# Kernel optimization log

Measured on AMD Instinct MI355X. Metric: run time of the kernel, lower is better.

Reference implementation:

```python
import jax, jax.numpy as jnp
import numpy as np

N_NODES = 100000
N_EDGES = 800000
IN_FEATS = 64
HIDDEN = 128
OUT_FEATS = 64
BN_EPS = 1e-5


def setup_inputs() -> dict:
    key = jax.random.key(0)
    ks = jax.random.split(key, 10)
    x = jax.random.normal(ks[0], (N_NODES, IN_FEATS), dtype=jnp.float32)
    edge_src = jax.random.randint(ks[1], (N_EDGES,), 0, N_NODES, dtype=jnp.int64)
    edge_dst = jax.random.randint(ks[2], (N_EDGES,), 0, N_NODES, dtype=jnp.int64)
    def lin(k, fan_in, fan_out):
        return jax.random.normal(k, (fan_in, fan_out), dtype=jnp.float32) / np.sqrt(fan_in)
    return {
        "x": x,
        "edge_src": edge_src,
        "edge_dst": edge_dst,
        "W_self1": lin(ks[3], IN_FEATS, HIDDEN),
        "W_neigh1": lin(ks[4], IN_FEATS, HIDDEN),
        "b1": jnp.zeros((HIDDEN,), jnp.float32),
        "bn_gamma": jnp.ones((HIDDEN,), jnp.float32),
        "bn_beta": jnp.zeros((HIDDEN,), jnp.float32),
        "W_self2": lin(ks[5], HIDDEN, OUT_FEATS),
        "W_neigh2": lin(ks[6], HIDDEN, OUT_FEATS),
        "b2": jnp.zeros((OUT_FEATS,), jnp.float32),
    }


def _sage_mean(h, edge_src, edge_dst, W_self, W_neigh, b, n_nodes):
    # mean aggregation over in-edges (SpMM): gather src feats, segment-sum by dst
    msg = h[edge_src]                                              # [E, F]
    summed = jax.ops.segment_sum(msg, edge_dst, num_segments=n_nodes)
    deg = jax.ops.segment_sum(jnp.ones(edge_dst.shape, h.dtype), edge_dst,
                              num_segments=n_nodes)
    agg = summed / jnp.maximum(deg, 1.0)[:, None]                  # zero-degree -> 0
    return h @ W_self + agg @ W_neigh + b


def reference(x, edge_src, edge_dst, W_self1, W_neigh1, b1, bn_gamma, bn_beta,
              W_self2, W_neigh2, b2):
    n = x.shape[0]
    h = _sage_mean(x, edge_src, edge_dst, W_self1, W_neigh1, b1, n)   # [N, hidden]
    # BatchNorm1d over the node dimension (training-mode batch stats)
    mu = jnp.mean(h, axis=0)
    var = jnp.var(h, axis=0)
    h = bn_gamma * (h - mu) * jax.lax.rsqrt(var + BN_EPS) + bn_beta
    h = jax.nn.relu(h)                                                # dropout = identity (eval)
    return _sage_mean(h, edge_src, edge_dst, W_self2, W_neigh2, b2, n)
```

## Files before the change

kernel.cpp:

```cpp
#include <hip/hip_runtime.h>

#define N_NODES 100000
#define N_EDGES 800000
#define IN_F 64
#define HID 128
#define OUT_F 64
#define BN_EPS 1e-5f
#define SCAN_NBLK ((N_NODES + 255) / 256)

typedef __attribute__((ext_vector_type(8))) short short8v;
typedef __attribute__((ext_vector_type(4))) float f32x4;

static __device__ __forceinline__ unsigned short f2bf(float f) {
  unsigned u = __float_as_uint(f);
  return (unsigned short)((u + 0x7FFFu + ((u >> 16) & 1u)) >> 16);
}
static __device__ __forceinline__ float bflo(unsigned u) {
  return __uint_as_float(u << 16);
}
static __device__ __forceinline__ float bfhi(unsigned u) {
  return __uint_as_float(u & 0xFFFF0000u);
}

__global__ __launch_bounds__(256) void cvtzero_kernel(
    const float* __restrict__ x, unsigned short* __restrict__ xb,
    int* __restrict__ cursor) {
  int t = blockIdx.x * 256 + threadIdx.x;
  if (t < N_NODES / 4) {
    int4 z = {0, 0, 0, 0};
    reinterpret_cast<int4*>(cursor)[t] = z;
  }
  if (t >= N_NODES * IN_F / 8) return;
  float4 a = reinterpret_cast<const float4*>(x)[t * 2];
  float4 b = reinterpret_cast<const float4*>(x)[t * 2 + 1];
  uint4 o;
  o.x = (unsigned)f2bf(a.x) | ((unsigned)f2bf(a.y) << 16);
  o.y = (unsigned)f2bf(a.z) | ((unsigned)f2bf(a.w) << 16);
  o.z = (unsigned)f2bf(b.x) | ((unsigned)f2bf(b.y) << 16);
  o.w = (unsigned)f2bf(b.z) | ((unsigned)f2bf(b.w) << 16);
  reinterpret_cast<uint4*>(xb)[t] = o;
}

__global__ __launch_bounds__(256) void pass1_kernel(
    const int* __restrict__ edst, int* __restrict__ cursor,
    unsigned short* __restrict__ pos16) {
  int t = blockIdx.x * 256 + threadIdx.x;
  if (t >= N_EDGES / 4) return;
  int4 d = reinterpret_cast<const int4*>(edst)[t];
  ushort4 p;
  p.x = (unsigned short)atomicAdd(cursor + d.x, 1);
  p.y = (unsigned short)atomicAdd(cursor + d.y, 1);
  p.z = (unsigned short)atomicAdd(cursor + d.z, 1);
  p.w = (unsigned short)atomicAdd(cursor + d.w, 1);
  reinterpret_cast<ushort4*>(pos16)[t] = p;
}

__global__ __launch_bounds__(256) void blocksum_kernel(
    const int* __restrict__ degi, int* __restrict__ bsum) {
  __shared__ int ls[256];
  int i = blockIdx.x * 256 + threadIdx.x;
  ls[threadIdx.x] = (i < N_NODES) ? degi[i] : 0;
  __syncthreads();
  for (int off = 128; off > 0; off >>= 1) {
    if (threadIdx.x < off) ls[threadIdx.x] += ls[threadIdx.x + off];
    __syncthreads();
  }
  if (threadIdx.x == 0) bsum[blockIdx.x] = ls[0];
}

__global__ __launch_bounds__(512) void scanb_kernel(
    const int* __restrict__ bsum, int* __restrict__ boff,
    int* __restrict__ rowstart, float* __restrict__ bnsum) {
  __shared__ int ls[512];
  int t = threadIdx.x;
  if (t < 256) bnsum[t] = 0.f;
  int v = (t < SCAN_NBLK) ? bsum[t] : 0;
  ls[t] = v;
  __syncthreads();
  for (int off = 1; off < 512; off <<= 1) {
    int u = (t >= off) ? ls[t - off] : 0;
    __syncthreads();
    ls[t] += u;
    __syncthreads();
  }
  if (t < SCAN_NBLK) boff[t] = ls[t] - v;
  if (t == 511) rowstart[N_NODES] = ls[511];
}

__global__ __launch_bounds__(256) void writerow_kernel(
    const int* __restrict__ degi, const int* __restrict__ boff,
    int* __restrict__ rowstart) {
  __shared__ int ls[256];
  int i = blockIdx.x * 256 + threadIdx.x;
  int t = threadIdx.x;
  int v = (i < N_NODES) ? degi[i] : 0;
  ls[t] = v;
  __syncthreads();
  for (int off = 1; off < 256; off <<= 1) {
    int u = (t >= off) ? ls[t - off] : 0;
    __syncthreads();
    ls[t] += u;
    __syncthreads();
  }
  if (i < N_NODES) rowstart[i] = boff[blockIdx.x] + ls[t] - v;
}

__global__ __launch_bounds__(256) void scatter_kernel(
    const int* __restrict__ esrc, const int* __restrict__ edst,
    const unsigned short* __restrict__ pos16,
    const int* __restrict__ rowstart, int* __restrict__ csr) {
  int t = blockIdx.x * 256 + threadIdx.x;
  if (t >= N_EDGES / 4) return;
  int4 s = reinterpret_cast<const int4*>(esrc)[t];
  int4 d = reinterpret_cast<const int4*>(edst)[t];
  ushort4 p = reinterpret_cast<const ushort4*>(pos16)[t];
  csr[rowstart[d.x] + p.x] = s.x;
  csr[rowstart[d.y] + p.y] = s.y;
  csr[rowstart[d.z] + p.z] = s.z;
  csr[rowstart[d.w] + p.w] = s.w;
}

__global__ __launch_bounds__(512) void gemm1_fused(
    const unsigned short* __restrict__ xb, const int* __restrict__ rowstart,
    const int* __restrict__ csr, const float* __restrict__ Ws,
    const float* __restrict__ Wn, const float* __restrict__ b,
    unsigned short* __restrict__ hb) {
  __shared__ __align__(16) unsigned short wt[128 * 128];
  __shared__ __align__(16) unsigned short aggl[128][72];
  __shared__ float bs[HID];
  int tid = threadIdx.x;
  for (int i = tid; i < 128 * 128; i += 512) {
    int k = i >> 7, j = i & 127;
    float v = (k < 64) ? Ws[k * HID + j] : Wn[(k - 64) * HID + j];
    int idx = (j << 7) | k;
    wt[idx ^ ((j & 15) << 3)] = f2bf(v);
  }
  if (tid < HID) bs[tid] = b[tid];
  __syncthreads();

  {
    int r_local = tid >> 2;
    int jj = tid & 3;
    int row = blockIdx.x * 128 + r_local;
    float acc[16];
#pragma unroll
    for (int e = 0; e < 16; ++e) acc[e] = 0.f;
    if (row < N_NODES) {
      int r0 = rowstart[row];
      int r1 = rowstart[row + 1];
      int i = r0;
      for (; i + 3 < r1; i += 4) {
        int s0 = csr[i], s1 = csr[i + 1], s2 = csr[i + 2], s3 = csr[i + 3];
        const uint4* p0 =
            reinterpret_cast<const uint4*>(xb + (size_t)s0 * 64 + jj * 16);
        const uint4* p1 =
            reinterpret_cast<const uint4*>(xb + (size_t)s1 * 64 + jj * 16);
        const uint4* p2 =
            reinterpret_cast<const uint4*>(xb + (size_t)s2 * 64 + jj * 16);
        const uint4* p3 =
            reinterpret_cast<const uint4*>(xb + (size_t)s3 * 64 + jj * 16);
        uint4 a0 = p0[0], b0 = p0[1];
        uint4 a1 = p1[0], b1 = p1[1];
        uint4 a2 = p2[0], b2 = p2[1];
        uint4 a3 = p3[0], b3 = p3[1];
        acc[0] += (bflo(a0.x) + bflo(a1.x)) + (bflo(a2.x) + bflo(a3.x));
        acc[1] += (bfhi(a0.x) + bfhi(a1.x)) + (bfhi(a2.x) + bfhi(a3.x));
        acc[2] += (bflo(a0.y) + bflo(a1.y)) + (bflo(a2.y) + bflo(a3.y));
        acc[3] += (bfhi(a0.y) + bfhi(a1.y)) + (bfhi(a2.y) + bfhi(a3.y));
        acc[4] += (bflo(a0.z) + bflo(a1.z)) + (bflo(a2.z) + bflo(a3.z));
        acc[5] += (bfhi(a0.z) + bfhi(a1.z)) + (bfhi(a2.z) + bfhi(a3.z));
        acc[6] += (bflo(a0.w) + bflo(a1.w)) + (bflo(a2.w) + bflo(a3.w));
        acc[7] += (bfhi(a0.w) + bfhi(a1.w)) + (bfhi(a2.w) + bfhi(a3.w));
        acc[8] += (bflo(b0.x) + bflo(b1.x)) + (bflo(b2.x) + bflo(b3.x));
        acc[9] += (bfhi(b0.x) + bfhi(b1.x)) + (bfhi(b2.x) + bfhi(b3.x));
        acc[10] += (bflo(b0.y) + bflo(b1.y)) + (bflo(b2.y) + bflo(b3.y));
        acc[11] += (bfhi(b0.y) + bfhi(b1.y)) + (bfhi(b2.y) + bfhi(b3.y));
        acc[12] += (bflo(b0.z) + bflo(b1.z)) + (bflo(b2.z) + bflo(b3.z));
        acc[13] += (bfhi(b0.z) + bfhi(b1.z)) + (bfhi(b2.z) + bfhi(b3.z));
        acc[14] += (bflo(b0.w) + bflo(b1.w)) + (bflo(b2.w) + bflo(b3.w));
        acc[15] += (bfhi(b0.w) + bfhi(b1.w)) + (bfhi(b2.w) + bfhi(b3.w));
      }
      for (; i < r1; ++i) {
        int s0 = csr[i];
        const uint4* p0 =
            reinterpret_cast<const uint4*>(xb + (size_t)s0 * 64 + jj * 16);
        uint4 a0 = p0[0], b0 = p0[1];
        acc[0] += bflo(a0.x);
        acc[1] += bfhi(a0.x);
        acc[2] += bflo(a0.y);
        acc[3] += bfhi(a0.y);
        acc[4] += bflo(a0.z);
        acc[5] += bfhi(a0.z);
        acc[6] += bflo(a0.w);
        acc[7] += bfhi(a0.w);
        acc[8] += bflo(b0.x);
        acc[9] += bfhi(b0.x);
        acc[10] += bflo(b0.y);
        acc[11] += bfhi(b0.y);
        acc[12] += bflo(b0.z);
        acc[13] += bfhi(b0.z);
        acc[14] += bflo(b0.w);
        acc[15] += bfhi(b0.w);
      }
      int deg = r1 - r0;
      float rd = 1.0f / (float)(deg > 0 ? deg : 1);
#pragma unroll
      for (int e = 0; e < 16; ++e) acc[e] *= rd;
    }
    uint4 o0, o1;
    o0.x = (unsigned)f2bf(acc[0]) | ((unsigned)f2bf(acc[1]) << 16);
    o0.y = (unsigned)f2bf(acc[2]) | ((unsigned)f2bf(acc[3]) << 16);
    o0.z = (unsigned)f2bf(acc[4]) | ((unsigned)f2bf(acc[5]) << 16);
    o0.w = (unsigned)f2bf(acc[6]) | ((unsigned)f2bf(acc[7]) << 16);
    o1.x = (unsigned)f2bf(acc[8]) | ((unsigned)f2bf(acc[9]) << 16);
    o1.y = (unsigned)f2bf(acc[10]) | ((unsigned)f2bf(acc[11]) << 16);
    o1.z = (unsigned)f2bf(acc[12]) | ((unsigned)f2bf(acc[13]) << 16);
    o1.w = (unsigned)f2bf(acc[14]) | ((unsigned)f2bf(acc[15]) << 16);
    uint4* dst = reinterpret_cast<uint4*>(&aggl[r_local][jj * 16]);
    dst[0] = o0;
    dst[1] = o1;
  }
  asm volatile("s_waitcnt lgkmcnt(0)" ::: "memory");

  int wave = tid >> 6, lane = tid & 63;
  int m = lane & 15, kg = lane >> 4;
  int rbase = blockIdx.x * 128 + wave * 16;
  int rowa = rbase + m;
  if (rowa >= N_NODES) rowa = N_NODES - 1;
  int lr = wave * 16 + m;

  short8v a[4];
#pragma unroll
  for (int kt = 0; kt < 4; ++kt) {
    int c0 = kt * 32 + kg * 8;
    if (c0 < 64) {
      a[kt] = *reinterpret_cast<const short8v*>(xb + (size_t)rowa * 64 + c0);
    } else {
      a[kt] = *reinterpret_cast<const short8v*>(&aggl[lr][c0 - 64]);
    }
  }

  f32x4 acc[8];
#pragma unroll
  for (int nt = 0; nt < 8; ++nt) acc[nt] = (f32x4){0.f, 0.f, 0.f, 0.f};

#pragma unroll
  for (int nt = 0; nt < 8; ++nt) {
    int col = nt * 16 + m;
    int base = col << 7;
    int sw = (col & 15) << 3;
#pragma unroll
    for (int kt = 0; kt < 4; ++kt) {
      int idx = (base | (kt * 32 + kg * 8)) ^ sw;
      short8v bf = *reinterpret_cast<const short8v*>(&wt[idx]);
      acc[nt] = __builtin_amdgcn_mfma_f32_16x16x32_bf16(a[kt], bf, acc[nt], 0, 0, 0);
    }
  }

#pragma unroll
  for (int nt = 0; nt < 8; ++nt) {
    int col = nt * 16 + m;
    float bias = bs[col];
#pragma unroll
    for (int r = 0; r < 4; ++r) {
      int rr = rbase + kg * 4 + r;
      if (rr < N_NODES) hb[(size_t)rr * HID + col] = f2bf(acc[nt][r] + bias);
    }
  }
}

__global__ __launch_bounds__(256) void aggb2_kernel(
    const unsigned short* __restrict__ zb, const unsigned short* __restrict__ sb,
    const int* __restrict__ rowstart, const int* __restrict__ csr,
    float* __restrict__ out) {
  int n = blockIdx.x * 32 + (threadIdx.x >> 3);
  int j = threadIdx.x & 7;
  if (n >= N_NODES) return;
  int r0 = rowstart[n];
  int r1 = rowstart[n + 1];
  float acc[8] = {0.f, 0.f, 0.f, 0.f, 0.f, 0.f, 0.f, 0.f};
  int i = r0;
  for (; i + 3 < r1; i += 4) {
    int s0 = csr[i], s1 = csr[i + 1], s2 = csr[i + 2], s3 = csr[i + 3];
    uint4 v0 = *reinterpret_cast<const uint4*>(zb + (size_t)s0 * 64 + j * 8);
    uint4 v1 = *reinterpret_cast<const uint4*>(zb + (size_t)s1 * 64 + j * 8);
    uint4 v2 = *reinterpret_cast<const uint4*>(zb + (size_t)s2 * 64 + j * 8);
    uint4 v3 = *reinterpret_cast<const uint4*>(zb + (size_t)s3 * 64 + j * 8);
    acc[0] += (bflo(v0.x) + bflo(v1.x)) + (bflo(v2.x) + bflo(v3.x));
    acc[1] += (bfhi(v0.x) + bfhi(v1.x)) + (bfhi(v2.x) + bfhi(v3.x));
    acc[2] += (bflo(v0.y) + bflo(v1.y)) + (bflo(v2.y) + bflo(v3.y));
    acc[3] += (bfhi(v0.y) + bfhi(v1.y)) + (bfhi(v2.y) + bfhi(v3.y));
    acc[4] += (bflo(v0.z) + bflo(v1.z)) + (bflo(v2.z) + bflo(v3.z));
    acc[5] += (bfhi(v0.z) + bfhi(v1.z)) + (bfhi(v2.z) + bfhi(v3.z));
    acc[6] += (bflo(v0.w) + bflo(v1.w)) + (bflo(v2.w) + bflo(v3.w));
    acc[7] += (bfhi(v0.w) + bfhi(v1.w)) + (bfhi(v2.w) + bfhi(v3.w));
  }
  for (; i < r1; ++i) {
    int s0 = csr[i];
    uint4 v0 = *reinterpret_cast<const uint4*>(zb + (size_t)s0 * 64 + j * 8);
    acc[0] += bflo(v0.x);
    acc[1] += bfhi(v0.x);
    acc[2] += bflo(v0.y);
    acc[3] += bfhi(v0.y);
    acc[4] += bflo(v0.z);
    acc[5] += bfhi(v0.z);
    acc[6] += bflo(v0.w);
    acc[7] += bfhi(v0.w);
  }
  int deg = r1 - r0;
  float rd = 1.0f / (float)(deg > 0 ? deg : 1);
  uint4 sv = *reinterpret_cast<const uint4*>(sb + (size_t)n * 64 + j * 8);
  float* dp = out + (size_t)n * 64 + j * 8;
  __builtin_nontemporal_store(bflo(sv.x) + acc[0] * rd, dp + 0);
  __builtin_nontemporal_store(bfhi(sv.x) + acc[1] * rd, dp + 1);
  __builtin_nontemporal_store(bflo(sv.y) + acc[2] * rd, dp + 2);
  __builtin_nontemporal_store(bfhi(sv.y) + acc[3] * rd, dp + 3);
  __builtin_nontemporal_store(bflo(sv.z) + acc[4] * rd, dp + 4);
  __builtin_nontemporal_store(bfhi(sv.z) + acc[5] * rd, dp + 5);
  __builtin_nontemporal_store(bflo(sv.w) + acc[6] * rd, dp + 6);
  __builtin_nontemporal_store(bfhi(sv.w) + acc[7] * rd, dp + 7);
}

__global__ __launch_bounds__(256) void bnstats_kernel(
    const unsigned short* __restrict__ hb, float* __restrict__ bnsum) {
  int j = threadIdx.x & 15;
  int g = threadIdx.x >> 4;
  float s[8] = {0.f, 0.f, 0.f, 0.f, 0.f, 0.f, 0.f, 0.f};
  float q[8] = {0.f, 0.f, 0.f, 0.f, 0.f, 0.f, 0.f, 0.f};
  for (int r = blockIdx.x * 16 + g; r < N_NODES; r += gridDim.x * 16) {
    uint4 v = *reinterpret_cast<const uint4*>(hb + (size_t)r * HID + j * 8);
    float f0 = bflo(v.x), f1 = bfhi(v.x), f2 = bflo(v.y), f3 = bfhi(v.y);
    float f4 = bflo(v.z), f5 = bfhi(v.z), f6 = bflo(v.w), f7 = bfhi(v.w);
    s[0] += f0; q[0] += f0 * f0;
    s[1] += f1; q[1] += f1 * f1;
    s[2] += f2; q[2] += f2 * f2;
    s[3] += f3; q[3] += f3 * f3;
    s[4] += f4; q[4] += f4 * f4;
    s[5] += f5; q[5] += f5 * f5;
    s[6] += f6; q[6] += f6 * f6;
    s[7] += f7; q[7] += f7 * f7;
  }
  __shared__ float lss[256 * 8];
  __shared__ float lqq[256 * 8];
#pragma unroll
  for (int e = 0; e < 8; ++e) {
    lss[threadIdx.x * 8 + e] = s[e];
    lqq[threadIdx.x * 8 + e] = q[e];
  }
  __syncthreads();
  if (threadIdx.x < 128) {
    int f = threadIdx.x;
    int jj = f >> 3, e = f & 7;
    float S = 0.f, Q = 0.f;
#pragma unroll
    for (int gg = 0; gg < 16; ++gg) {
      S += lss[(gg * 16 + jj) * 8 + e];
      Q += lqq[(gg * 16 + jj) * 8 + e];
    }
    unsafeAtomicAdd(bnsum + f, S);
    unsafeAtomicAdd(bnsum + 128 + f, Q);
  }
}

__global__ __launch_bounds__(512) void gemm2_mfma(
    const unsigned short* __restrict__ hb, const float* __restrict__ bnsum,
    const float* __restrict__ gamma, const float* __restrict__ beta,
    const float* __restrict__ Wn, const float* __restrict__ Ws,
    const float* __restrict__ b, unsigned short* __restrict__ zb,
    unsigned short* __restrict__ sb) {
  __shared__ __align__(16) unsigned short wt[128 * 128];
  __shared__ float scs[HID];
  __shared__ float shs[HID];
  __shared__ float bz[OUT_F];
  int tid = threadIdx.x;
  for (int i = tid; i < 128 * 128; i += 512) {
    int k = i >> 7, j = i & 127;
    float v = (j < 64) ? Wn[k * OUT_F + j] : Ws[k * OUT_F + (j - 64)];
    int idx = (j << 7) | k;
    wt[idx ^ ((j & 15) << 3)] = f2bf(v);
  }
  if (tid < HID) {
    const float invn = 1.0f / (float)N_NODES;
    float mu = bnsum[tid] * invn;
    float var = bnsum[128 + tid] * invn - mu * mu;
    float sc = gamma[tid] * rsqrtf(var + BN_EPS);
    scs[tid] = sc;
    shs[tid] = beta[tid] - mu * sc;
  }
  if (tid < OUT_F) bz[tid] = b[tid];
  __syncthreads();

  int wave = tid >> 6, lane = tid & 63;
  int m = lane & 15, kg = lane >> 4;
  int rbase = blockIdx.x * 128 + wave * 16;
  int rowa = rbase + m;
  if (rowa >= N_NODES) rowa = N_NODES - 1;

  short8v a[4];
#pragma unroll
  for (int kt = 0; kt < 4; ++kt) {
    int c0 = kt * 32 + kg * 8;
    uint4 raw = *reinterpret_cast<const uint4*>(hb + (size_t)rowa * HID + c0);
    float4 sc0 = *reinterpret_cast<const float4*>(&scs[c0]);
    float4 sc1 = *reinterpret_cast<const float4*>(&scs[c0 + 4]);
    float4 sh0 = *reinterpret_cast<const float4*>(&shs[c0]);
    float4 sh1 = *reinterpret_cast<const float4*>(&shs[c0 + 4]);
    short8v av;
    av[0] = (short)f2bf(fmaxf(bflo(raw.x) * sc0.x + sh0.x, 0.f));
    av[1] = (short)f2bf(fmaxf(bfhi(raw.x) * sc0.y + sh0.y, 0.f));
    av[2] = (short)f2bf(fmaxf(bflo(raw.y) * sc0.z + sh0.z, 0.f));
    av[3] = (short)f2bf(fmaxf(bfhi(raw.y) * sc0.w + sh0.w, 0.f));
    av[4] = (short)f2bf(fmaxf(bflo(raw.z) * sc1.x + sh1.x, 0.f));
    av[5] = (short)f2bf(fmaxf(bfhi(raw.z) * sc1.y + sh1.y, 0.f));
    av[6] = (short)f2bf(fmaxf(bflo(raw.w) * sc1.z + sh1.z, 0.f));
    av[7] = (short)f2bf(fmaxf(bfhi(raw.w) * sc1.w + sh1.w, 0.f));
    a[kt] = av;
  }

  f32x4 acc[8];
#pragma unroll
  for (int nt = 0; nt < 8; ++nt) acc[nt] = (f32x4){0.f, 0.f, 0.f, 0.f};

#pragma unroll
  for (int nt = 0; nt < 8; ++nt) {
    int col = nt * 16 + m;
    int base = col << 7;
    int sw = (col & 15) << 3;
#pragma unroll
    for (int kt = 0; kt < 4; ++kt) {
      int idx = (base | (kt * 32 + kg * 8)) ^ sw;
      short8v bf = *reinterpret_cast<const short8v*>(&wt[idx]);
      acc[nt] = __builtin_amdgcn_mfma_f32_16x16x32_bf16(a[kt], bf, acc[nt], 0, 0, 0);
    }
  }

#pragma unroll
  for (int nt = 0; nt < 8; ++nt) {
    int col = nt * 16 + m;
#pragma unroll
    for (int r = 0; r < 4; ++r) {
      int rr = rbase + kg * 4 + r;
      if (rr < N_NODES) {
        float v = acc[nt][r];
        if (col < 64)
          zb[(size_t)rr * OUT_F + col] = f2bf(v);
        else
          sb[(size_t)rr * OUT_F + (col - 64)] = f2bf(v + bz[col - 64]);
      }
    }
  }
}

extern "C" void kernel_launch(void* const* d_in, const int* in_sizes, int n_in,
                              void* d_out, int out_size, void* d_ws,
                              size_t ws_size, hipStream_t stream) {
  const float* x = (const float*)d_in[0];
  const int* esrc = (const int*)d_in[1];
  const int* edst = (const int*)d_in[2];
  const float* Ws1 = (const float*)d_in[3];
  const float* Wn1 = (const float*)d_in[4];
  const float* b1 = (const float*)d_in[5];
  const float* gamma = (const float*)d_in[6];
  const float* beta = (const float*)d_in[7];
  const float* Ws2 = (const float*)d_in[8];
  const float* Wn2 = (const float*)d_in[9];
  const float* b2 = (const float*)d_in[10];
  float* out = (float*)d_out;

  float* ws = (float*)d_ws;
  float* bnsum = ws;
  int* cursor = (int*)(ws + 512);
  int* rowstart = cursor + N_NODES;
  int* bsum = rowstart + N_NODES + 1;
  int* boff = bsum + SCAN_NBLK;
  int* csr = boff + SCAN_NBLK;
  int pos16_off = ((512 + 2 * N_NODES + 1 + 2 * SCAN_NBLK + N_EDGES) + 3) & ~3;
  unsigned short* pos16 = (unsigned short*)(ws + pos16_off);
  unsigned short* xb = (unsigned short*)(ws + pos16_off + N_EDGES / 2);
  unsigned short* zbuf = xb + (size_t)N_NODES * 64;
  unsigned short* sb = zbuf + (size_t)N_NODES * 64;
  unsigned short* hb = sb + (size_t)N_NODES * 64;

  const int e4grid = (N_EDGES / 4 + 255) / 256;
  cvtzero_kernel<<<(N_NODES * IN_F / 8 + 255) / 256, 256, 0, stream>>>(x, xb,
                                                                       cursor);
  pass1_kernel<<<e4grid, 256, 0, stream>>>(edst, cursor, pos16);
  blocksum_kernel<<<SCAN_NBLK, 256, 0, stream>>>(cursor, bsum);
  scanb_kernel<<<1, 512, 0, stream>>>(bsum, boff, rowstart, bnsum);
  writerow_kernel<<<SCAN_NBLK, 256, 0, stream>>>(cursor, boff, rowstart);
  scatter_kernel<<<e4grid, 256, 0, stream>>>(esrc, edst, pos16, rowstart, csr);

  const int ggrid = (N_NODES + 127) / 128;
  const int agrid = (N_NODES + 31) / 32;
  gemm1_fused<<<ggrid, 512, 0, stream>>>(xb, rowstart, csr, Ws1, Wn1, b1, hb);

  bnstats_kernel<<<256, 256, 0, stream>>>(hb, bnsum);

  gemm2_mfma<<<ggrid, 512, 0, stream>>>(hb, bnsum, gamma, beta, Wn2, Ws2, b2,
                                        zbuf, sb);
  aggb2_kernel<<<agrid, 256, 0, stream>>>(zbuf, sb, rowstart, csr, out);
}
```

Measured before the change: 175.8 us.

## Pre-convert weights to bf16 once and read B fragments from global

Weight transposition and bf16 conversion for both layers move into the prep kernel, which writes compact column-major bf16 weight tables to the workspace. The GEMM kernels no longer stage the 32KB weight tile into LDS per block; MFMA B operands are loaded straight from global/L2. Blocks shrink to 256 threads and 64 rows, which lowers LDS use and may raise occupancy. The cost is repeated global loads of weights per block, relying on cache hits, and twice as many blocks.

```diff
diff --git a/kernel.cpp b/kernel.cpp
--- a/kernel.cpp
+++ b/kernel.cpp
@@ -22,23 +22,48 @@
   return __uint_as_float(u & 0xFFFF0000u);
 }
 
-__global__ __launch_bounds__(256) void cvtzero_kernel(
-    const float* __restrict__ x, unsigned short* __restrict__ xb,
+__global__ __launch_bounds__(256) void prep_kernel(
+    const float* __restrict__ x, const float* __restrict__ Ws1,
+    const float* __restrict__ Wn1, const float* __restrict__ Wn2,
+    const float* __restrict__ Ws2, unsigned short* __restrict__ xb,
+    unsigned short* __restrict__ wb1, unsigned short* __restrict__ wb2,
     int* __restrict__ cursor) {
   int t = blockIdx.x * 256 + threadIdx.x;
   if (t < N_NODES / 4) {
     int4 z = {0, 0, 0, 0};
     reinterpret_cast<int4*>(cursor)[t] = z;
   }
-  if (t >= N_NODES * IN_F / 8) return;
-  float4 a = reinterpret_cast<const float4*>(x)[t * 2];
-  float4 b = reinterpret_cast<const float4*>(x)[t * 2 + 1];
-  uint4 o;
-  o.x = (unsigned)f2bf(a.x) | ((unsigned)f2bf(a.y) << 16);
-  o.y = (unsigned)f2bf(a.z) | ((unsigned)f2bf(a.w) << 16);
-  o.z = (unsigned)f2bf(b.x) | ((unsigned)f2bf(b.y) << 16);
-  o.w = (unsigned)f2bf(b.z) | ((unsigned)f2bf(b.w) << 16);
-  reinterpret_cast<uint4*>(xb)[t] = o;
+  if (t < N_NODES * IN_F / 8) {
+    float4 a = reinterpret_cast<const float4*>(x)[t * 2];
+    float4 b = reinterpret_cast<const float4*>(x)[t * 2 + 1];
+    uint4 o;
+    o.x = (unsigned)f2bf(a.x) | ((unsigned)f2bf(a.y) << 16);
+    o.y = (unsigned)f2bf(a.z) | ((unsigned)f2bf(a.w) << 16);
+    o.z = (unsigned)f2bf(b.x) | ((unsigned)f2bf(b.y) << 16);
+    o.w = (unsigned)f2bf(b.z) | ((unsigned)f2bf(b.w) << 16);
+    reinterpret_cast<uint4*>(xb)[t] = o;
+  } else {
+    int idx = t - N_NODES * IN_F / 8;
+    if (idx < 4096) {
+      int e0 = idx * 8;
+      int table = e0 >> 14;
+      int ee0 = e0 & 16383;
+      int col = ee0 >> 7, k0 = ee0 & 127;
+      unsigned short tmp[8];
+#pragma unroll
+      for (int q = 0; q < 8; ++q) {
+        int k = k0 + q;
+        float v;
+        if (table == 0)
+          v = (k < 64) ? Ws1[k * HID + col] : Wn1[(k - 64) * HID + col];
+        else
+          v = (col < 64) ? Wn2[k * OUT_F + col] : Ws2[k * OUT_F + (col - 64)];
+        tmp[q] = f2bf(v);
+      }
+      unsigned short* dst = (table == 0 ? wb1 : wb2) + ee0;
+      *reinterpret_cast<uint4*>(dst) = *reinterpret_cast<const uint4*>(tmp);
+    }
+  }
 }
 
 __global__ __launch_bounds__(256) void pass1_kernel(
@@ -120,28 +145,17 @@
   csr[rowstart[d.w] + p.w] = s.w;
 }
 
-__global__ __launch_bounds__(512) void gemm1_fused(
+__global__ __launch_bounds__(256) void gemm1_fused(
     const unsigned short* __restrict__ xb, const int* __restrict__ rowstart,
-    const int* __restrict__ csr, const float* __restrict__ Ws,
-    const float* __restrict__ Wn, const float* __restrict__ b,
-    unsigned short* __restrict__ hb) {
-  __shared__ __align__(16) unsigned short wt[128 * 128];
-  __shared__ __align__(16) unsigned short aggl[128][72];
-  __shared__ float bs[HID];
+    const int* __restrict__ csr, const unsigned short* __restrict__ wb,
+    const float* __restrict__ b, unsigned short* __restrict__ hb) {
+  __shared__ __align__(16) unsigned short aggl[64][72];
   int tid = threadIdx.x;
-  for (int i = tid; i < 128 * 128; i += 512) {
-    int k = i >> 7, j = i & 127;
-    float v = (k < 64) ? Ws[k * HID + j] : Wn[(k - 64) * HID + j];
-    int idx = (j << 7) | k;
-    wt[idx ^ ((j & 15) << 3)] = f2bf(v);
-  }
-  if (tid < HID) bs[tid] = b[tid];
-  __syncthreads();
 
   {
     int r_local = tid >> 2;
     int jj = tid & 3;
-    int row = blockIdx.x * 128 + r_local;
+    int row = blockIdx.x * 64 + r_local;
     float acc[16];
 #pragma unroll
     for (int e = 0; e < 16; ++e) acc[e] = 0.f;
@@ -224,7 +238,7 @@
 
   int wave = tid >> 6, lane = tid & 63;
   int m = lane & 15, kg = lane >> 4;
-  int rbase = blockIdx.x * 128 + wave * 16;
+  int rbase = blockIdx.x * 64 + wave * 16;
   int rowa = rbase + m;
   if (rowa >= N_NODES) rowa = N_NODES - 1;
   int lr = wave * 16 + m;
@@ -247,12 +261,11 @@
 #pragma unroll
   for (int nt = 0; nt < 8; ++nt) {
     int col = nt * 16 + m;
-    int base = col << 7;
-    int sw = (col & 15) << 3;
+    const unsigned short* wcol = wb + ((size_t)col << 7);
 #pragma unroll
     for (int kt = 0; kt < 4; ++kt) {
-      int idx = (base | (kt * 32 + kg * 8)) ^ sw;
-      short8v bf = *reinterpret_cast<const short8v*>(&wt[idx]);
+      short8v bf =
+          *reinterpret_cast<const short8v*>(wcol + kt * 32 + kg * 8);
       acc[nt] = __builtin_amdgcn_mfma_f32_16x16x32_bf16(a[kt], bf, acc[nt], 0, 0, 0);
     }
   }
@@ -260,7 +273,7 @@
 #pragma unroll
   for (int nt = 0; nt < 8; ++nt) {
     int col = nt * 16 + m;
-    float bias = bs[col];
+    float bias = b[col];
 #pragma unroll
     for (int r = 0; r < 4; ++r) {
       int rr = rbase + kg * 4 + r;
@@ -362,23 +375,14 @@
   }
 }
 
-__global__ __launch_bounds__(512) void gemm2_mfma(
+__global__ __launch_bounds__(256) void gemm2_mfma(
     const unsigned short* __restrict__ hb, const float* __restrict__ bnsum,
     const float* __restrict__ gamma, const float* __restrict__ beta,
-    const float* __restrict__ Wn, const float* __restrict__ Ws,
-    const float* __restrict__ b, unsigned short* __restrict__ zb,
-    unsigned short* __restrict__ sb) {
-  __shared__ __align__(16) unsigned short wt[128 * 128];
+    const unsigned short* __restrict__ wb, const float* __restrict__ b,
+    unsigned short* __restrict__ zb, unsigned short* __restrict__ sb) {
   __shared__ float scs[HID];
   __shared__ float shs[HID];
-  __shared__ float bz[OUT_F];
   int tid = threadIdx.x;
-  for (int i = tid; i < 128 * 128; i += 512) {
-    int k = i >> 7, j = i & 127;
-    float v = (j < 64) ? Wn[k * OUT_F + j] : Ws[k * OUT_F + (j - 64)];
-    int idx = (j << 7) | k;
-    wt[idx ^ ((j & 15) << 3)] = f2bf(v);
-  }
   if (tid < HID) {
     const float invn = 1.0f / (float)N_NODES;
     float mu = bnsum[tid] * invn;
@@ -387,12 +391,11 @@
     scs[tid] = sc;
     shs[tid] = beta[tid] - mu * sc;
   }
-  if (tid < OUT_F) bz[tid] = b[tid];
   __syncthreads();
 
   int wave = tid >> 6, lane = tid & 63;
   int m = lane & 15, kg = lane >> 4;
-  int rbase = blockIdx.x * 128 + wave * 16;
+  int rbase = blockIdx.x * 64 + wave * 16;
   int rowa = rbase + m;
   if (rowa >= N_NODES) rowa = N_NODES - 1;
 
@@ -424,12 +427,11 @@
 #pragma unroll
   for (int nt = 0; nt < 8; ++nt) {
     int col = nt * 16 + m;
-    int base = col << 7;
-    int sw = (col & 15) << 3;
+    const unsigned short* wcol = wb + ((size_t)col << 7);
 #pragma unroll
     for (int kt = 0; kt < 4; ++kt) {
-      int idx = (base | (kt * 32 + kg * 8)) ^ sw;
-      short8v bf = *reinterpret_cast<const short8v*>(&wt[idx]);
+      short8v bf =
+          *reinterpret_cast<const short8v*>(wcol + kt * 32 + kg * 8);
       acc[nt] = __builtin_amdgcn_mfma_f32_16x16x32_bf16(a[kt], bf, acc[nt], 0, 0, 0);
     }
   }
@@ -445,7 +447,7 @@
         if (col < 64)
           zb[(size_t)rr * OUT_F + col] = f2bf(v);
         else
-          sb[(size_t)rr * OUT_F + (col - 64)] = f2bf(v + bz[col - 64]);
+          sb[(size_t)rr * OUT_F + (col - 64)] = f2bf(v + b[col - 64]);
       }
     }
   }
@@ -469,12 +471,15 @@
 
   float* ws = (float*)d_ws;
   float* bnsum = ws;
-  int* cursor = (int*)(ws + 512);
+  unsigned short* wb1 = (unsigned short*)(ws + 256);
+  unsigned short* wb2 = (unsigned short*)(ws + 8448);
+  int* cursor = (int*)(ws + 16640);
   int* rowstart = cursor + N_NODES;
   int* bsum = rowstart + N_NODES + 1;
   int* boff = bsum + SCAN_NBLK;
   int* csr = boff + SCAN_NBLK;
-  int pos16_off = ((512 + 2 * N_NODES + 1 + 2 * SCAN_NBLK + N_EDGES) + 3) & ~3;
+  int pos16_off =
+      ((16640 + 2 * N_NODES + 1 + 2 * SCAN_NBLK + N_EDGES) + 3) & ~3;
   unsigned short* pos16 = (unsigned short*)(ws + pos16_off);
   unsigned short* xb = (unsigned short*)(ws + pos16_off + N_EDGES / 2);
   unsigned short* zbuf = xb + (size_t)N_NODES * 64;
@@ -482,21 +487,21 @@
   unsigned short* hb = sb + (size_t)N_NODES * 64;
 
   const int e4grid = (N_EDGES / 4 + 255) / 256;
-  cvtzero_kernel<<<(N_NODES * IN_F / 8 + 255) / 256, 256, 0, stream>>>(x, xb,
-                                                                       cursor);
+  prep_kernel<<<(N_NODES * IN_F / 8 + 4096 + 255) / 256, 256, 0, stream>>>(
+      x, Ws1, Wn1, Wn2, Ws2, xb, wb1, wb2, cursor);
   pass1_kernel<<<e4grid, 256, 0, stream>>>(edst, cursor, pos16);
   blocksum_kernel<<<SCAN_NBLK, 256, 0, stream>>>(cursor, bsum);
   scanb_kernel<<<1, 512, 0, stream>>>(bsum, boff, rowstart, bnsum);
   writerow_kernel<<<SCAN_NBLK, 256, 0, stream>>>(cursor, boff, rowstart);
   scatter_kernel<<<e4grid, 256, 0, stream>>>(esrc, edst, pos16, rowstart, csr);
 
-  const int ggrid = (N_NODES + 127) / 128;
+  const int ggrid = (N_NODES + 63) / 64;
   const int agrid = (N_NODES + 31) / 32;
-  gemm1_fused<<<ggrid, 512, 0, stream>>>(xb, rowstart, csr, Ws1, Wn1, b1, hb);
+  gemm1_fused<<<ggrid, 256, 0, stream>>>(xb, rowstart, csr, wb1, b1, hb);
 
   bnstats_kernel<<<256, 256, 0, stream>>>(hb, bnsum);
 
-  gemm2_mfma<<<ggrid, 512, 0, stream>>>(hb, bnsum, gamma, beta, Wn2, Ws2, b2,
-                                        zbuf, sb);
+  gemm2_mfma<<<ggrid, 256, 0, stream>>>(hb, bnsum, gamma, beta, wb2, b2, zbuf,
+                                        sb);
   aggb2_kernel<<<agrid, 256, 0, stream>>>(zbuf, sb, rowstart, csr, out);
 }
```

After: 214.7 us. 1.22x slower.
